# Performance work log

Hardware: AMD Instinct MI355X
Metric: run time of the kernel (lower is better)

The kernel has to match this reference:

```python
import jax, jax.numpy as jnp
import numpy as np

B, S = 128, 64          # batch, sequence length (cities)
H = 128                 # hidden size
STATIC, DYNAMIC = 2, 2  # static/dynamic feature channels


def setup_inputs() -> dict:
    key = jax.random.key(0)
    ks = jax.random.split(key, 16)
    g = lambda k, shape: (jax.random.normal(k, shape, dtype=jnp.float32) * 0.1)
    return {
        "static": jax.random.normal(ks[0], (B, STATIC, S), dtype=jnp.float32),
        "dynamic": jax.random.uniform(ks[1], (B, DYNAMIC, S), dtype=jnp.float32),
        "x0": jnp.zeros((STATIC,), jnp.float32),           # learned initial decoder input
        "static_w": g(ks[2], (H, STATIC)),  "static_b": g(ks[3], (H,)),
        "dynamic_w": g(ks[4], (H, DYNAMIC)), "dynamic_b": g(ks[5], (H,)),
        "decoder_w": g(ks[6], (H, STATIC)), "decoder_b": g(ks[7], (H,)),
        "gru_wih": g(ks[8], (3 * H, H)), "gru_whh": g(ks[9], (3 * H, H)),
        "gru_bih": g(ks[10], (3 * H,)), "gru_bhh": g(ks[11], (3 * H,)),
        "attn_v": g(ks[12], (H,)), "attn_W": g(ks[13], (H, 3 * H)),
        "ptr_v": g(ks[14], (H,)),  "ptr_W": g(ks[15], (H, 2 * H)),
    }


def _forward(static, dynamic, x0, static_w, static_b, dynamic_w, dynamic_b,
             decoder_w, decoder_b, gru_wih, gru_whh, gru_bih, gru_bhh,
             attn_v, attn_W, ptr_v, ptr_W):
    Bsz, in_size, seq = static.shape
    # Conv1d with kernel_size=1 == pointwise channel mixing
    conv = lambda w, b, x: jnp.einsum('oi,bis->bos', w, x) + b[None, :, None]
    static_h = conv(static_w, static_b, static)      # [B,H,S]
    dynamic_h = conv(dynamic_w, dynamic_b, dynamic)  # [B,H,S]

    def gru_cell(x, h):
        # torch nn.GRU gate order: r, z, n
        gi = x @ gru_wih.T + gru_bih
        gh = h @ gru_whh.T + gru_bhh
        i_r, i_z, i_n = jnp.split(gi, 3, axis=1)
        h_r, h_z, h_n = jnp.split(gh, 3, axis=1)
        r = jax.nn.sigmoid(i_r + h_r)
        z = jax.nn.sigmoid(i_z + h_z)
        n = jnp.tanh(i_n + r * h_n)
        return (1.0 - z) * n + z * h

    def step(carry, _):
        dec_in, h = carry                                   # [B,in,1], [B,H]
        dec_h = conv(decoder_w, decoder_b, dec_in)[:, :, 0]  # [B,H]
        h_new = gru_cell(dec_h, h)                           # rnn_out == last_hh (1 layer)
        rnn_out = h_new
        # encoder attention over cities
        hid = jnp.concatenate(
            [static_h, dynamic_h,
             jnp.broadcast_to(rnn_out[:, :, None], static_h.shape)], axis=1)  # [B,3H,S]
        e = jnp.tanh(jnp.einsum('hk,bks->bhs', attn_W, hid))
        attns = jax.nn.softmax(jnp.einsum('h,bhs->bs', attn_v, e), axis=1)    # [B,S]
        context = jnp.einsum('bs,bhs->bh', attns, static_h)                   # [B,H]
        energy = jnp.concatenate(
            [static_h, jnp.broadcast_to(context[:, :, None], static_h.shape)], axis=1)
        logits = jnp.einsum('h,bhs->bs', ptr_v,
                            jnp.tanh(jnp.einsum('hk,bks->bhs', ptr_W, energy)))
        # mask_fn is None -> mask stays all ones -> mask.log() == 0
        logp_all = jax.nn.log_softmax(logits, axis=1)
        ptr = jnp.argmax(logp_all, axis=1)                  # greedy (eval mode)
        logp = jnp.take_along_axis(logp_all, ptr[:, None], axis=1)[:, 0]
        idx = jnp.broadcast_to(ptr[:, None, None], (Bsz, in_size, 1))
        new_in = jax.lax.stop_gradient(jnp.take_along_axis(static, idx, axis=2))
        return (new_in, h_new), (ptr, logp)

    dec0 = jnp.broadcast_to(x0[None, :, None], (Bsz, in_size, 1))
    h0 = jnp.zeros((Bsz, static_h.shape[1]), static.dtype)
    _, (ptrs, logps) = jax.lax.scan(step, (dec0, h0), None, length=seq)
    return ptrs.T, logps.T  # tour_idx [B,S] int, tour_logp [B,S] float


def reference(static, dynamic, x0, static_w, static_b, dynamic_w, dynamic_b,
              decoder_w, decoder_b, gru_wih, gru_whh, gru_bih, gru_bhh,
              attn_v, attn_W, ptr_v, ptr_W):
    return _forward(static, dynamic, x0, static_w, static_b, dynamic_w, dynamic_b,
                    decoder_w, decoder_b, gru_wih, gru_whh, gru_bih, gru_bhh,
                    attn_v, attn_W, ptr_v, ptr_W)
```

## Files before the change

kernel.cpp:

```cpp
#include <hip/hip_runtime.h>
#include <math.h>


#define K1  1.44269504088896340736f
#define K2  2.88539008177792681472f
#define LN2 0.69314718055994530942f

#define WS_M     0
#define WS_C     768
#define WS_PREA  1152
#define WS_PREP  (WS_PREA + 128*8192)
#define WS_Q     (WS_PREP + 128*8192)

template <int CTRL>
__device__ __forceinline__ float dppk(float x) {
  int xi = __builtin_bit_cast(int, x);
  return __builtin_bit_cast(float,
      __builtin_amdgcn_update_dpp(xi, xi, CTRL, 0xF, 0xF, false));
}
template <int CTRL>
__device__ __forceinline__ float dppz(float x) {
  int xi = __builtin_bit_cast(int, x);
  return __builtin_bit_cast(float,
      __builtin_amdgcn_update_dpp(0, xi, CTRL, 0xF, 0xF, true));
}
__device__ __forceinline__ float bcastf(float x, int lane) {
  return __builtin_bit_cast(float,
      __builtin_amdgcn_readlane(__builtin_bit_cast(int, x), lane));
}
__device__ __forceinline__ float sum4(float x) {
  x += dppk<0xB1>(x); x += dppk<0x4E>(x); return x;
}
__device__ __forceinline__ float sum8(float x) {
  x += dppk<0xB1>(x); x += dppk<0x4E>(x); x += dppk<0x141>(x); return x;
}
__device__ __forceinline__ float wsum64(float x) {
  x += dppz<0x111>(x); x += dppz<0x112>(x); x += dppz<0x114>(x);
  x += dppz<0x118>(x); x += dppz<0x142>(x); x += dppz<0x143>(x);
  return bcastf(x, 63);
}
__device__ __forceinline__ float wmax64(float x) {
  x = fmaxf(x, dppk<0x111>(x)); x = fmaxf(x, dppk<0x112>(x));
  x = fmaxf(x, dppk<0x114>(x)); x = fmaxf(x, dppk<0x118>(x));
  x = fmaxf(x, dppk<0x142>(x)); x = fmaxf(x, dppk<0x143>(x));
  return bcastf(x, 63);
}
#define RCP(x)  __builtin_amdgcn_rcpf(x)
#define EXP2(x) __builtin_amdgcn_exp2f(x)

__device__ __forceinline__ void bar_lds() {
  asm volatile("s_waitcnt lgkmcnt(0)" ::: "memory");
  __builtin_amdgcn_s_barrier();
  asm volatile("" ::: "memory");
}

__device__ __forceinline__ int rot8(int p) {
  return (p & 56) | ((p + (p >> 3)) & 7);
}

__global__ __launch_bounds__(256) void prep_small(
    const float* __restrict__ wih, const float* __restrict__ decw,
    const float* __restrict__ decb, const float* __restrict__ bih,
    float* __restrict__ ws) {
  int gid = blockIdx.x * 256 + threadIdx.x;
  if (gid < 384) {
    float m0 = 0.f, m1 = 0.f, cc = 0.f;
    for (int k = 0; k < 128; ++k) {
      float w = wih[gid * 128 + k];
      m0 += w * decw[k * 2 + 0];
      m1 += w * decw[k * 2 + 1];
      cc += w * decb[k];
    }
    ws[WS_M + gid * 2 + 0] = m0;
    ws[WS_M + gid * 2 + 1] = m1;
    ws[WS_C + gid] = cc + bih[gid];
  }
}

__global__ __launch_bounds__(256) void prep_big(
    const float* __restrict__ statics, const float* __restrict__ dynamics,
    const float* __restrict__ sw, const float* __restrict__ sb,
    const float* __restrict__ dw, const float* __restrict__ db,
    const float* __restrict__ attn_W, const float* __restrict__ ptr_W,
    float* __restrict__ ws) {
  __shared__ __align__(16) float sh[128 * 64];
  __shared__ __align__(16) float dh[128 * 64];
  __shared__ float st[128];
  __shared__ float dy[128];
  int b = blockIdx.x >> 3;
  int hq = blockIdx.x & 7;
  int t = threadIdx.x;
  if (t < 128) st[t] = statics[b * 128 + t];
  else         dy[t - 128] = dynamics[b * 128 + (t - 128)];
  __syncthreads();
  for (int e = t; e < 8192; e += 256) {
    int h = e >> 6, s = e & 63;
    sh[e] = sw[h * 2 + 0] * st[s] + sw[h * 2 + 1] * st[64 + s] + sb[h];
    dh[e] = dw[h * 2 + 0] * dy[s] + dw[h * 2 + 1] * dy[64 + s] + db[h];
  }
  __syncthreads();
  int hh = hq * 16 + (t >> 4);
  int s0 = (t & 15) * 4;
  float4 pA = {0, 0, 0, 0}, pP = {0, 0, 0, 0}, qq = {0, 0, 0, 0};
  for (int k = 0; k < 128; ++k) {
    float4 sv = *(const float4*)&sh[k * 64 + s0];
    float4 dv = *(const float4*)&dh[k * 64 + s0];
    float w1 = attn_W[hh * 384 + k];
    float w2 = attn_W[hh * 384 + 128 + k];
    float p1 = ptr_W[hh * 256 + k];
    float p2 = ptr_W[hh * 256 + 128 + k];
    pA.x += w1 * sv.x + w2 * dv.x;  pA.y += w1 * sv.y + w2 * dv.y;
    pA.z += w1 * sv.z + w2 * dv.z;  pA.w += w1 * sv.w + w2 * dv.w;
    pP.x += p1 * sv.x;  pP.y += p1 * sv.y;  pP.z += p1 * sv.z;  pP.w += p1 * sv.w;
    qq.x += p2 * sv.x;  qq.y += p2 * sv.y;  qq.z += p2 * sv.z;  qq.w += p2 * sv.w;
  }
  float4 eA, eP;
  eA.x = exp2f(K2 * pA.x); eA.y = exp2f(K2 * pA.y);
  eA.z = exp2f(K2 * pA.z); eA.w = exp2f(K2 * pA.w);
  eP.x = exp2f(K2 * pP.x); eP.y = exp2f(K2 * pP.y);
  eP.z = exp2f(K2 * pP.z); eP.w = exp2f(K2 * pP.w);
  int o = b * 8192 + hh * 64 + s0;
  *(float4*)&ws[WS_PREA + o] = eA;
  *(float4*)&ws[WS_PREP + o] = eP;
  *(float4*)&ws[WS_Q + o]    = qq;
}

__global__ __launch_bounds__(512)
__attribute__((amdgpu_waves_per_eu(2)))
void drl4tsp_main(
    const float* __restrict__ statics, const float* __restrict__ x0,
    const float* __restrict__ whh, const float* __restrict__ attn_W,
    const float* __restrict__ bhh_g, const float* __restrict__ attn_v,
    const float* __restrict__ ptr_v, const float* __restrict__ ws,
    float* __restrict__ out) {
  __shared__ float4 W3s4[128 * 32];
  __shared__ float4 EAT4[64 * 32];
  __shared__ float4 EPT4[64 * 32];
  __shared__ float4 uav3[64];
  __shared__ float4 uav2[64];
  __shared__ float4 gp4[128 * 3];
  __shared__ __align__(16) float hp[144];
  __shared__ __align__(16) float attns[64];
  __shared__ float a_lds[64];
  __shared__ float l_lds[64];
  __shared__ float stt[128];
  __shared__ float outbuf[64];
  __shared__ float Lhist[4096];

  const int b    = blockIdx.x;
  const int t    = threadIdx.x;
  const int lane = t & 63;
  const int g    = t >> 2;
  const int q    = t & 3;
  const int s    = t >> 3;
  const int hg   = t & 7;

  float wr0[32], wr1[32], wr2[32];
#pragma unroll
  for (int kk = 0; kk < 8; ++kk) {
    float4 a = *(const float4*)(whh + g * 128         + kk * 16 + q * 4);
    float4 c = *(const float4*)(whh + (128 + g) * 128 + kk * 16 + q * 4);
    float4 d = *(const float4*)(whh + (256 + g) * 128 + kk * 16 + q * 4);
    wr0[4*kk] = a.x; wr0[4*kk+1] = a.y; wr0[4*kk+2] = a.z; wr0[4*kk+3] = a.w;
    wr1[4*kk] = c.x; wr1[4*kk+1] = c.y; wr1[4*kk+2] = c.z; wr1[4*kk+3] = c.w;
    wr2[4*kk] = d.x; wr2[4*kk+1] = d.y; wr2[4*kk+2] = d.z; wr2[4*kk+3] = d.w;
  }
  float qr[16];
  {
    const float4* pq = (const float4*)(ws + WS_Q + b * 8192 + g * 64 + q * 16);
#pragma unroll
    for (int i = 0; i < 4; ++i) {
      float4 v = pq[i];
      qr[4*i] = v.x; qr[4*i+1] = v.y; qr[4*i+2] = v.z; qr[4*i+3] = v.w;
    }
  }

  {
    const float4* src = (const float4*)(attn_W + g * 384 + 256);
#pragma unroll
    for (int kk = 0; kk < 8; ++kk) {
      int j = q * 8 + kk;
      W3s4[g * 32 + ((j + g) & 31)] = src[j];
    }
  }
  for (int e = t; e < 8192; e += 512) {
    int h = e >> 6, sE = e & 63;
    int rg = ((h >> 2) + sE) & 31;
    ((float*)EAT4)[sE * 128 + rg * 4 + (h & 3)] = ws[WS_PREA + b * 8192 + e];
    ((float*)EPT4)[sE * 128 + rg * 4 + (h & 3)] = ws[WS_PREP + b * 8192 + e];
  }
  if (t < 128) {
    int h = t;
    int rg = rot8(h >> 1);
    ((float*)uav3)[rg * 4 + (h & 1) * 2 + 1] = 2.0f * attn_v[h];
    ((float*)uav2)[rg * 4 + (h & 1) * 2 + 1] = 2.0f * ptr_v[h];
    stt[h] = statics[b * 128 + h];
    const float* Mm = ws + WS_M;
    const float* Cc = ws + WS_C;
    float cR = Cc[h] + bhh_g[h];
    float cZ = Cc[128 + h] + bhh_g[128 + h];
    gp4[h*3 + 0] = float4{Mm[h*2], Mm[h*2+1], cR, Mm[(128+h)*2]};
    gp4[h*3 + 1] = float4{Mm[(128+h)*2+1], cZ, Mm[(256+h)*2], Mm[(256+h)*2+1]};
    gp4[h*3 + 2] = float4{Cc[256+h], bhh_g[256+h], 0.f, 0.f};
  }
  __syncthreads();

  float hreg = 0.f, ghr = 0.f, ghz = 0.f, ghn = 0.f;
  float d0 = x0[0], d1 = x0[1];

  for (int step = 0; step < 64; ++step) {
    {
      float4 v0 = gp4[g*3], v1 = gp4[g*3+1], v2 = gp4[g*3+2];
      float r = RCP(1.f + EXP2(-K1 * (v0.x*d0 + v0.y*d1 + v0.z + ghr)));
      float z = RCP(1.f + EXP2(-K1 * (v0.w*d0 + v1.x*d1 + v1.y + ghz)));
      float xn = v1.z*d0 + v1.w*d1 + v2.x + r * (ghn + v2.y);
      float n = 1.f - 2.f * RCP(EXP2(K2 * xn) + 1.f);
      hreg = (1.f - z) * n + z * hreg;
      if (q == 0) hp[(g >> 5) * 36 + (g & 31)] = hreg;
    }
    bar_lds();
    {
      float u3a = 0.f, u3b = 0.f;
#pragma unroll
      for (int kk = 0; kk < 8; ++kk) {
        float4 hv = *(const float4*)&hp[(kk >> 1) * 36 + (kk & 1) * 16 + q * 4];
        float4 wv = W3s4[g * 32 + ((kk * 4 + q + g) & 31)];
        float d2 = wv.x*hv.x + wv.y*hv.y + wv.z*hv.z + wv.w*hv.w;
        if (kk & 1) u3b += d2; else u3a += d2;
      }
      float u3 = sum4(u3a + u3b);
      if (q == 0)
        ((float*)uav3)[rot8(g >> 1) * 4 + (g & 1) * 2] = EXP2(K2 * u3);
    }
    bar_lds();
    float sr = 0.f, sz = 0.f, sn = 0.f;
    {
      float acc0 = 0.f, acc1 = 0.f;
#pragma unroll
      for (int ii = 0; ii < 4; ++ii) {
        float4 ea = EAT4[s * 32 + ((hg * 4 + ii + s) & 31)];
        int p0 = hg * 8 + 2 * ii;
        float4 ua = uav3[(p0 & 56) | ((p0 + hg) & 7)];
        float4 ub = uav3[((p0+1) & 56) | ((p0 + 1 + hg) & 7)];
        float x1 = ea.x * ua.x + 1.f, y1 = ea.y * ua.z + 1.f;
        acc0 += (ua.y * y1 + ua.w * x1) * RCP(x1 * y1);
        float x2 = ea.z * ub.x + 1.f, y2 = ea.w * ub.z + 1.f;
        acc1 += (ub.y * y2 + ub.w * x2) * RCP(x2 * y2);
      }
#pragma unroll
      for (int kk = 0; kk < 4; ++kk) {
        float4 hv = *(const float4*)&hp[(kk >> 1) * 36 + (kk & 1) * 16 + q * 4];
        int k = kk * 4;
        sr += wr0[k]*hv.x + wr0[k+1]*hv.y + wr0[k+2]*hv.z + wr0[k+3]*hv.w;
        sz += wr1[k]*hv.x + wr1[k+1]*hv.y + wr1[k+2]*hv.z + wr1[k+3]*hv.w;
        sn += wr2[k]*hv.x + wr2[k+1]*hv.y + wr2[k+2]*hv.z + wr2[k+3]*hv.w;
      }
      float acc = sum8(acc0 + acc1);
      if (hg == 0) a_lds[s] = -acc;
    }
    bar_lds();
    float4 ep0, ep1, ep2, ep3;
    {
      float a = a_lds[lane];
      ep0 = EPT4[s * 32 + ((hg * 4 + 0 + s) & 31)];
      ep1 = EPT4[s * 32 + ((hg * 4 + 1 + s) & 31)];
      ep2 = EPT4[s * 32 + ((hg * 4 + 2 + s) & 31)];
      ep3 = EPT4[s * 32 + ((hg * 4 + 3 + s) & 31)];
      float e = EXP2(K1 * a);
      attns[lane] = e;
#pragma unroll
      for (int kk = 4; kk < 8; ++kk) {
        float4 hv = *(const float4*)&hp[(kk >> 1) * 36 + (kk & 1) * 16 + q * 4];
        int k = kk * 4;
        sr += wr0[k]*hv.x + wr0[k+1]*hv.y + wr0[k+2]*hv.z + wr0[k+3]*hv.w;
        sz += wr1[k]*hv.x + wr1[k+1]*hv.y + wr1[k+2]*hv.z + wr1[k+3]*hv.w;
        sn += wr2[k]*hv.x + wr2[k+1]*hv.y + wr2[k+2]*hv.z + wr2[k+3]*hv.w;
      }
      float sum = wsum64(e);
      float p = 0.f;
#pragma unroll
      for (int ii = 0; ii < 4; ++ii) {
        float4 av = *(const float4*)&attns[q * 16 + ii * 4];
        p += qr[4*ii]*av.x + qr[4*ii+1]*av.y + qr[4*ii+2]*av.z + qr[4*ii+3]*av.w;
      }
      p *= RCP(sum);
      p = sum4(p);
      if (q == 0)
        ((float*)uav2)[rot8(g >> 1) * 4 + (g & 1) * 2] = EXP2(K2 * p);
      ghr = sum4(sr); ghz = sum4(sz); ghn = sum4(sn);
    }
    bar_lds();
    {
      float acc0 = 0.f, acc1 = 0.f;
#pragma unroll
      for (int ii = 0; ii < 4; ++ii) {
        float4 ep = (ii == 0) ? ep0 : (ii == 1) ? ep1 : (ii == 2) ? ep2 : ep3;
        int p0 = hg * 8 + 2 * ii;
        float4 ua = uav2[(p0 & 56) | ((p0 + hg) & 7)];
        float4 ub = uav2[((p0+1) & 56) | ((p0 + 1 + hg) & 7)];
        float x1 = ep.x * ua.x + 1.f, y1 = ep.y * ua.z + 1.f;
        acc0 += (ua.y * y1 + ua.w * x1) * RCP(x1 * y1);
        float x2 = ep.z * ub.x + 1.f, y2 = ep.w * ub.z + 1.f;
        acc1 += (ub.y * y2 + ub.w * x2) * RCP(x2 * y2);
      }
      float acc = sum8(acc0 + acc1);
      if (hg == 0) l_lds[s] = -acc;
    }
    bar_lds();
    {
      float L = l_lds[lane];
      float v = wmax64(L);
      unsigned long long mk = __ballot(L == v);
      int idx = __builtin_ctzll(mk);
      if (t < 64) Lhist[step * 64 + t] = L;
      if (t == 0) outbuf[step] = (float)idx;
      d0 = stt[idx];
      d1 = stt[64 + idx];
    }
  }
  bar_lds();
  {
    int wv = t >> 6;
    for (int st = wv; st < 64; st += 8) {
      float L = Lhist[st * 64 + lane];
      float v = wmax64(L);
      float e2 = EXP2(K1 * (L - v));
      float s3 = wsum64(e2);
      if (lane == 0)
        out[8192 + b * 64 + st] = -LN2 * __builtin_amdgcn_logf(s3);
      if (lane == 1)
        out[b * 64 + st] = outbuf[st];
    }
  }
}

extern "C" void kernel_launch(void* const* d_in, const int* in_sizes, int n_in,
                              void* d_out, int out_size, void* d_ws, size_t ws_size,
                              hipStream_t stream) {
  const float* statics  = (const float*)d_in[0];
  const float* dynamics = (const float*)d_in[1];
  const float* x0       = (const float*)d_in[2];
  const float* sw       = (const float*)d_in[3];
  const float* sb       = (const float*)d_in[4];
  const float* dw       = (const float*)d_in[5];
  const float* db       = (const float*)d_in[6];
  const float* decw     = (const float*)d_in[7];
  const float* decb     = (const float*)d_in[8];
  const float* wih      = (const float*)d_in[9];
  const float* whh      = (const float*)d_in[10];
  const float* bih      = (const float*)d_in[11];
  const float* bhh      = (const float*)d_in[12];
  const float* attn_v   = (const float*)d_in[13];
  const float* attn_W   = (const float*)d_in[14];
  const float* ptr_v    = (const float*)d_in[15];
  const float* ptr_W    = (const float*)d_in[16];
  float* ws  = (float*)d_ws;
  float* out = (float*)d_out;

  hipLaunchKernelGGL(prep_small, dim3(2), dim3(256), 0, stream,
                     wih, decw, decb, bih, ws);
  hipLaunchKernelGGL(prep_big, dim3(1024), dim3(256), 0, stream,
                     statics, dynamics, sw, sb, dw, db, attn_W, ptr_W, ws);
  hipLaunchKernelGGL(drl4tsp_main, dim3(128), dim3(512), 0, stream,
                     statics, x0, whh, attn_W, bhh, attn_v, ptr_v, ws, out);
}
```

Before: 202.8 us.

## Restructure attention/pointer energy work split and merge GRU matvec into single phase

Moves the whole hidden-state GRU matvec (sr/sz/sn) into the same loop as the attention u3 projection, instead of spreading it across two later phases. Re-lays the precomputed attention and pointer energies as h-pair-major rows with padding. The energy reductions now have each lane own an h-pair and each wave cover eight sequence positions, with a new DPP/shuffle merge4 cross-lane reduction in place of the per-thread rotated-index float4 loads. The log-softmax sum is computed inside the step loop instead of replaying a 4096-entry history buffer at the end, which cuts LDS use. The trade-off is more cross-lane shuffles per step and a different per-step instruction mix and schedule.

```diff
diff --git a/kernel.cpp b/kernel.cpp
--- a/kernel.cpp
+++ b/kernel.cpp
@@ -31,9 +31,6 @@
 __device__ __forceinline__ float sum4(float x) {
   x += dppk<0xB1>(x); x += dppk<0x4E>(x); return x;
 }
-__device__ __forceinline__ float sum8(float x) {
-  x += dppk<0xB1>(x); x += dppk<0x4E>(x); x += dppk<0x141>(x); return x;
-}
 __device__ __forceinline__ float wsum64(float x) {
   x += dppz<0x111>(x); x += dppz<0x112>(x); x += dppz<0x114>(x);
   x += dppz<0x118>(x); x += dppz<0x142>(x); x += dppz<0x143>(x);
@@ -54,8 +51,18 @@
   asm volatile("" ::: "memory");
 }
 
-__device__ __forceinline__ int rot8(int p) {
-  return (p & 56) | ((p + (p >> 3)) & 7);
+__device__ __forceinline__ float merge4(float a0, float a1, float a2, float a3,
+                                        int lane) {
+  float m0 = a0 + dppk<0xB1>(a0), m1 = a1 + dppk<0xB1>(a1);
+  float m2 = a2 + dppk<0xB1>(a2), m3 = a3 + dppk<0xB1>(a3);
+  float s01 = (lane & 1) ? m1 : m0, s23 = (lane & 1) ? m3 : m2;
+  float n0 = s01 + dppk<0x4E>(s01), n1 = s23 + dppk<0x4E>(s23);
+  float v = (lane & 2) ? n1 : n0;
+  v += dppk<0x128>(v);
+  v += __shfl_xor(v, 4);
+  v += __shfl_xor(v, 16);
+  v += __shfl_xor(v, 32);
+  return v;
 }
 
 __global__ __launch_bounds__(256) void prep_small(
@@ -134,8 +141,8 @@
     const float* __restrict__ ptr_v, const float* __restrict__ ws,
     float* __restrict__ out) {
   __shared__ float4 W3s4[128 * 32];
-  __shared__ float4 EAT4[64 * 32];
-  __shared__ float4 EPT4[64 * 32];
+  __shared__ __align__(16) float EAI[64 * 132];
+  __shared__ __align__(16) float EPI[64 * 132];
   __shared__ float4 uav3[64];
   __shared__ float4 uav2[64];
   __shared__ float4 gp4[128 * 3];
@@ -145,15 +152,14 @@
   __shared__ float l_lds[64];
   __shared__ float stt[128];
   __shared__ float outbuf[64];
-  __shared__ float Lhist[4096];
+  __shared__ float s3buf[64];
 
   const int b    = blockIdx.x;
   const int t    = threadIdx.x;
   const int lane = t & 63;
+  const int wv   = t >> 6;
   const int g    = t >> 2;
   const int q    = t & 3;
-  const int s    = t >> 3;
-  const int hg   = t & 7;
 
   float wr0[32], wr1[32], wr2[32];
 #pragma unroll
@@ -185,15 +191,14 @@
   }
   for (int e = t; e < 8192; e += 512) {
     int h = e >> 6, sE = e & 63;
-    int rg = ((h >> 2) + sE) & 31;
-    ((float*)EAT4)[sE * 128 + rg * 4 + (h & 3)] = ws[WS_PREA + b * 8192 + e];
-    ((float*)EPT4)[sE * 128 + rg * 4 + (h & 3)] = ws[WS_PREP + b * 8192 + e];
+    int dst = (h >> 1) * 132 + (h & 1) * 64 + sE;
+    EAI[dst] = ws[WS_PREA + b * 8192 + e];
+    EPI[dst] = ws[WS_PREP + b * 8192 + e];
   }
   if (t < 128) {
     int h = t;
-    int rg = rot8(h >> 1);
-    ((float*)uav3)[rg * 4 + (h & 1) * 2 + 1] = 2.0f * attn_v[h];
-    ((float*)uav2)[rg * 4 + (h & 1) * 2 + 1] = 2.0f * ptr_v[h];
+    ((float*)uav3)[(h >> 1) * 4 + (h & 1) * 2 + 1] = 2.0f * attn_v[h];
+    ((float*)uav2)[(h >> 1) * 4 + (h & 1) * 2 + 1] = 2.0f * ptr_v[h];
     stt[h] = statics[b * 128 + h];
     const float* Mm = ws + WS_M;
     const float* Cc = ws + WS_C;
@@ -220,62 +225,53 @@
     }
     bar_lds();
     {
-      float u3a = 0.f, u3b = 0.f;
+      float u3 = 0.f, sr = 0.f, sz = 0.f, sn = 0.f;
 #pragma unroll
       for (int kk = 0; kk < 8; ++kk) {
         float4 hv = *(const float4*)&hp[(kk >> 1) * 36 + (kk & 1) * 16 + q * 4];
         float4 wv = W3s4[g * 32 + ((kk * 4 + q + g) & 31)];
-        float d2 = wv.x*hv.x + wv.y*hv.y + wv.z*hv.z + wv.w*hv.w;
-        if (kk & 1) u3b += d2; else u3a += d2;
-      }
-      float u3 = sum4(u3a + u3b);
-      if (q == 0)
-        ((float*)uav3)[rot8(g >> 1) * 4 + (g & 1) * 2] = EXP2(K2 * u3);
-    }
-    bar_lds();
-    float sr = 0.f, sz = 0.f, sn = 0.f;
-    {
-      float acc0 = 0.f, acc1 = 0.f;
-#pragma unroll
-      for (int ii = 0; ii < 4; ++ii) {
-        float4 ea = EAT4[s * 32 + ((hg * 4 + ii + s) & 31)];
-        int p0 = hg * 8 + 2 * ii;
-        float4 ua = uav3[(p0 & 56) | ((p0 + hg) & 7)];
-        float4 ub = uav3[((p0+1) & 56) | ((p0 + 1 + hg) & 7)];
-        float x1 = ea.x * ua.x + 1.f, y1 = ea.y * ua.z + 1.f;
-        acc0 += (ua.y * y1 + ua.w * x1) * RCP(x1 * y1);
-        float x2 = ea.z * ub.x + 1.f, y2 = ea.w * ub.z + 1.f;
-        acc1 += (ub.y * y2 + ub.w * x2) * RCP(x2 * y2);
-      }
-#pragma unroll
-      for (int kk = 0; kk < 4; ++kk) {
-        float4 hv = *(const float4*)&hp[(kk >> 1) * 36 + (kk & 1) * 16 + q * 4];
         int k = kk * 4;
+        u3 += wv.x*hv.x + wv.y*hv.y + wv.z*hv.z + wv.w*hv.w;
         sr += wr0[k]*hv.x + wr0[k+1]*hv.y + wr0[k+2]*hv.z + wr0[k+3]*hv.w;
         sz += wr1[k]*hv.x + wr1[k+1]*hv.y + wr1[k+2]*hv.z + wr1[k+3]*hv.w;
         sn += wr2[k]*hv.x + wr2[k+1]*hv.y + wr2[k+2]*hv.z + wr2[k+3]*hv.w;
       }
-      float acc = sum8(acc0 + acc1);
-      if (hg == 0) a_lds[s] = -acc;
-    }
-    bar_lds();
-    float4 ep0, ep1, ep2, ep3;
+      ghr = sum4(sr); ghz = sum4(sz); ghn = sum4(sn);
+      u3 = sum4(u3);
+      if (q == 0)
+        ((float*)uav3)[(g >> 1) * 4 + (g & 1) * 2] = EXP2(K2 * u3);
+    }
+    bar_lds();
+    {
+      float4 uv = uav3[lane];
+      const float* rowA = &EAI[lane * 132 + 8 * wv];
+      const float* rowB = rowA + 64;
+      float o0, o1;
+#pragma unroll
+      for (int pass = 0; pass < 2; ++pass) {
+        float4 eaA = *(const float4*)(rowA + 4 * pass);
+        float a0 = uv.y * RCP(eaA.x * uv.x + 1.f);
+        float a1 = uv.y * RCP(eaA.y * uv.x + 1.f);
+        float a2 = uv.y * RCP(eaA.z * uv.x + 1.f);
+        float a3 = uv.y * RCP(eaA.w * uv.x + 1.f);
+        float4 eaB = *(const float4*)(rowB + 4 * pass);
+        a0 += uv.w * RCP(eaB.x * uv.z + 1.f);
+        a1 += uv.w * RCP(eaB.y * uv.z + 1.f);
+        a2 += uv.w * RCP(eaB.z * uv.z + 1.f);
+        a3 += uv.w * RCP(eaB.w * uv.z + 1.f);
+        float m = merge4(a0, a1, a2, a3, lane);
+        if (pass == 0) o0 = m; else o1 = m;
+      }
+      if (lane < 4) {
+        a_lds[8 * wv + lane]     = -o0;
+        a_lds[8 * wv + 4 + lane] = -o1;
+      }
+    }
+    bar_lds();
     {
       float a = a_lds[lane];
-      ep0 = EPT4[s * 32 + ((hg * 4 + 0 + s) & 31)];
-      ep1 = EPT4[s * 32 + ((hg * 4 + 1 + s) & 31)];
-      ep2 = EPT4[s * 32 + ((hg * 4 + 2 + s) & 31)];
-      ep3 = EPT4[s * 32 + ((hg * 4 + 3 + s) & 31)];
       float e = EXP2(K1 * a);
       attns[lane] = e;
-#pragma unroll
-      for (int kk = 4; kk < 8; ++kk) {
-        float4 hv = *(const float4*)&hp[(kk >> 1) * 36 + (kk & 1) * 16 + q * 4];
-        int k = kk * 4;
-        sr += wr0[k]*hv.x + wr0[k+1]*hv.y + wr0[k+2]*hv.z + wr0[k+3]*hv.w;
-        sz += wr1[k]*hv.x + wr1[k+1]*hv.y + wr1[k+2]*hv.z + wr1[k+3]*hv.w;
-        sn += wr2[k]*hv.x + wr2[k+1]*hv.y + wr2[k+2]*hv.z + wr2[k+3]*hv.w;
-      }
       float sum = wsum64(e);
       float p = 0.f;
 #pragma unroll
@@ -286,25 +282,33 @@
       p *= RCP(sum);
       p = sum4(p);
       if (q == 0)
-        ((float*)uav2)[rot8(g >> 1) * 4 + (g & 1) * 2] = EXP2(K2 * p);
-      ghr = sum4(sr); ghz = sum4(sz); ghn = sum4(sn);
-    }
-    bar_lds();
-    {
-      float acc0 = 0.f, acc1 = 0.f;
-#pragma unroll
-      for (int ii = 0; ii < 4; ++ii) {
-        float4 ep = (ii == 0) ? ep0 : (ii == 1) ? ep1 : (ii == 2) ? ep2 : ep3;
-        int p0 = hg * 8 + 2 * ii;
-        float4 ua = uav2[(p0 & 56) | ((p0 + hg) & 7)];
-        float4 ub = uav2[((p0+1) & 56) | ((p0 + 1 + hg) & 7)];
-        float x1 = ep.x * ua.x + 1.f, y1 = ep.y * ua.z + 1.f;
-        acc0 += (ua.y * y1 + ua.w * x1) * RCP(x1 * y1);
-        float x2 = ep.z * ub.x + 1.f, y2 = ep.w * ub.z + 1.f;
-        acc1 += (ub.y * y2 + ub.w * x2) * RCP(x2 * y2);
-      }
-      float acc = sum8(acc0 + acc1);
-      if (hg == 0) l_lds[s] = -acc;
+        ((float*)uav2)[(g >> 1) * 4 + (g & 1) * 2] = EXP2(K2 * p);
+    }
+    bar_lds();
+    {
+      float4 uv = uav2[lane];
+      const float* rowA = &EPI[lane * 132 + 8 * wv];
+      const float* rowB = rowA + 64;
+      float o0, o1;
+#pragma unroll
+      for (int pass = 0; pass < 2; ++pass) {
+        float4 epA = *(const float4*)(rowA + 4 * pass);
+        float a0 = uv.y * RCP(epA.x * uv.x + 1.f);
+        float a1 = uv.y * RCP(epA.y * uv.x + 1.f);
+        float a2 = uv.y * RCP(epA.z * uv.x + 1.f);
+        float a3 = uv.y * RCP(epA.w * uv.x + 1.f);
+        float4 epB = *(const float4*)(rowB + 4 * pass);
+        a0 += uv.w * RCP(epB.x * uv.z + 1.f);
+        a1 += uv.w * RCP(epB.y * uv.z + 1.f);
+        a2 += uv.w * RCP(epB.z * uv.z + 1.f);
+        a3 += uv.w * RCP(epB.w * uv.z + 1.f);
+        float m = merge4(a0, a1, a2, a3, lane);
+        if (pass == 0) o0 = m; else o1 = m;
+      }
+      if (lane < 4) {
+        l_lds[8 * wv + lane]     = -o0;
+        l_lds[8 * wv + 4 + lane] = -o1;
+      }
     }
     bar_lds();
     {
@@ -312,26 +316,22 @@
       float v = wmax64(L);
       unsigned long long mk = __ballot(L == v);
       int idx = __builtin_ctzll(mk);
-      if (t < 64) Lhist[step * 64 + t] = L;
-      if (t == 0) outbuf[step] = (float)idx;
+      float e2 = EXP2(K1 * (L - v));
+      float s3 = wsum64(e2);
+      if (t == 0) {
+        outbuf[step] = (float)idx;
+        s3buf[step] = s3;
+      }
       d0 = stt[idx];
       d1 = stt[64 + idx];
     }
   }
   bar_lds();
-  {
-    int wv = t >> 6;
-    for (int st = wv; st < 64; st += 8) {
-      float L = Lhist[st * 64 + lane];
-      float v = wmax64(L);
-      float e2 = EXP2(K1 * (L - v));
-      float s3 = wsum64(e2);
-      if (lane == 0)
-        out[8192 + b * 64 + st] = -LN2 * __builtin_amdgcn_logf(s3);
-      if (lane == 1)
-        out[b * 64 + st] = outbuf[st];
-    }
-  }
+  if (t < 64)
+    out[b * 64 + t] = outbuf[t];
+  else if (t < 128)
+    out[8192 + b * 64 + (t - 64)] =
+        -LN2 * __builtin_amdgcn_logf(s3buf[t - 64]);
 }
 
 extern "C" void kernel_launch(void* const* d_in, const int* in_sizes, int n_in,
```

New measurement: 228.1 us. 1.12x slower.
